# Optimization experiments

Hardware: AMD Instinct MI355X
Metric: run time of the kernel (lower is better)

The kernel has to match this reference:

```python
import jax, jax.numpy as jnp
import numpy as np

CAPACITY_FACTOR = 1.25

def setup_inputs() -> dict:
    key = jax.random.key(0)
    ks = jax.random.split(key, 6)
    B, S, D, H, E = 4, 2048, 1024, 2048, 8
    x = jax.random.normal(ks[0], (B, S, D), dtype=jnp.float32)
    Wg = jax.random.normal(ks[1], (D, E), dtype=jnp.float32) / np.float32(np.sqrt(D))
    bg = jnp.zeros((E,), dtype=jnp.float32)
    W1 = jax.random.normal(ks[2], (E, H, D), dtype=jnp.float32) / np.float32(np.sqrt(H))
    W2 = jax.random.normal(ks[3], (E, D, H), dtype=jnp.float32) / np.float32(np.sqrt(D))
    W3 = jax.random.normal(ks[4], (E, D, H), dtype=jnp.float32) / np.float32(np.sqrt(D))
    return {"x": x, "Wg": Wg, "bg": bg, "W1": W1, "W2": W2, "W3": W3, "deterministic": 1}


def reference(x, Wg, bg, W1, W2, W3, deterministic):
    # deterministic=True path: no gate noise, no dropout (rate=0 anyway).
    b, s, d = x.shape
    E = W1.shape[0]
    xt = x.reshape(-1, d)                      # [N, d]
    N = xt.shape[0]
    cap = int(N / E * CAPACITY_FACTOR)

    logits = xt @ Wg + bg                      # [N, E]
    eid = jnp.argmax(logits, axis=1)           # [N] assigned expert (top-1)
    onehot = jax.nn.one_hot(eid, E, dtype=xt.dtype)
    # 0-based arrival position of each token within its expert's queue
    pos = (jnp.sum(jnp.cumsum(onehot, axis=0) * onehot, axis=1)).astype(jnp.int32) - 1
    valid = pos < cap                          # capacity mask (pos >= 0 always)
    slot = jnp.where(valid, pos, cap)          # overflow tokens -> dummy slot `cap`

    # Dispatch: scatter tokens into [E, cap+1, d]; slots unique among valid tokens
    buf = jnp.zeros((E, cap + 1, d), dtype=xt.dtype).at[eid, slot].set(xt)
    binp = buf[:, :cap]                        # [E, cap, d] (dummy slot dropped)

    # Grouped SwiGLU FFN per expert
    h = jax.nn.silu(jnp.einsum('ecd,edh->ech', binp, W2)) * jnp.einsum('ecd,edh->ech', binp, W3)
    bout = jnp.einsum('ech,ehd->ecd', h, W1)   # [E, cap, d]

    # Combine: gather each token's expert output; overflow tokens read zero row
    bout = jnp.concatenate([bout, jnp.zeros((E, 1, d), dtype=bout.dtype)], axis=1)
    eout = bout[eid, slot]                     # [N, d]

    weights = jax.nn.softmax(logits, axis=-1)
    gate_w = jnp.take_along_axis(weights, eid[:, None], axis=1)  # [N, 1]
    out = (gate_w * eout).reshape(b, s, d)
    return out
```

## Files before the change

### kernel.cpp

```cpp
#include <hip/hip_runtime.h>

#define N_TOK 8192
#define D_DIM 1024
#define H_DIM 2048
#define E_NUM 8
#define CAP   1280

typedef __attribute__((ext_vector_type(8))) short bf16x8;
typedef __attribute__((ext_vector_type(8))) unsigned short u16x8;
typedef __attribute__((ext_vector_type(4))) float f32x4;

__device__ inline unsigned short f2bf(float f) {
  unsigned u = __float_as_uint(f);
  u += 0x7fffu + ((u >> 16) & 1u);
  return (unsigned short)(u >> 16);
}

__device__ inline void vm_drain() {
  asm volatile("s_waitcnt vmcnt(0)" ::: "memory");
}

__global__ __launch_bounds__(256) void transpose_cvt(const float* __restrict__ src,
                                                     unsigned short* __restrict__ dst,
                                                     int R, int C) {
  __shared__ float tile[64][33];
  const int b = blockIdx.z;
  src += (size_t)b * R * C;
  dst += (size_t)b * R * C;
  const int c0 = blockIdx.x * 32, r0 = blockIdx.y * 64;
  const int tx = threadIdx.x & 31, ty = threadIdx.x >> 5;
#pragma unroll
  for (int i = 0; i < 8; ++i)
    tile[ty + i * 8][tx] = src[(size_t)(r0 + ty + i * 8) * C + c0 + tx];
  __syncthreads();
  const int rp = threadIdx.x & 31;
  const int cb = threadIdx.x >> 5;
#pragma unroll
  for (int it = 0; it < 4; ++it) {
    const int c = cb + it * 8;
    unsigned short v[2] = {f2bf(tile[2 * rp][c]), f2bf(tile[2 * rp + 1][c])};
    *reinterpret_cast<unsigned*>(dst + (size_t)(c0 + c) * R + r0 + 2 * rp) =
        *reinterpret_cast<unsigned*>(v);
  }
}

__global__ __launch_bounds__(256) void gate_kernel(const float* __restrict__ x,
                                                   const float* __restrict__ Wg,
                                                   const float* __restrict__ bg,
                                                   int* __restrict__ eid,
                                                   float* __restrict__ gatew) {
  __shared__ float wg[E_NUM][D_DIM];
  const int tid = threadIdx.x;
  for (int i = tid; i < D_DIM * E_NUM; i += 256) {
    int d = i >> 3, e = i & 7;
    wg[e][d] = Wg[i];
  }
  __syncthreads();
  const int w = tid >> 6, l = tid & 63;
  const int t = blockIdx.x * 4 + w;
  const float* xr = x + (size_t)t * D_DIM;
  float acc[8] = {0, 0, 0, 0, 0, 0, 0, 0};
#pragma unroll
  for (int i = 0; i < D_DIM / 64; ++i) {
    float xv = xr[l + 64 * i];
#pragma unroll
    for (int e = 0; e < 8; ++e) acc[e] += xv * wg[e][l + 64 * i];
  }
#pragma unroll
  for (int off = 32; off >= 1; off >>= 1) {
#pragma unroll
    for (int e = 0; e < 8; ++e) acc[e] += __shfl_xor(acc[e], off);
  }
  if (l == 0) {
    float best = -1e30f;
    int bi = 0;
#pragma unroll
    for (int e = 0; e < 8; ++e) {
      acc[e] += bg[e];
      if (acc[e] > best) { best = acc[e]; bi = e; }
    }
    float s = 0.f;
#pragma unroll
    for (int e = 0; e < 8; ++e) s += __expf(acc[e] - best);
    eid[t] = bi;
    gatew[t] = 1.f / s;
  }
}

__global__ void init_tok(int* __restrict__ tok_of) {
  int i = blockIdx.x * 256 + threadIdx.x;
  if (i < E_NUM * CAP) tok_of[i] = -1;
}

__global__ void scan_kernel(const int* __restrict__ eid, int* __restrict__ slot,
                            int* __restrict__ tok_of) {
  __shared__ int se[N_TOK];
  const int tid = threadIdx.x;
  for (int i = tid; i < N_TOK; i += 256) se[i] = eid[i];
  __syncthreads();
  if (tid >= 64) return;
  int counts[8] = {0, 0, 0, 0, 0, 0, 0, 0};
  const unsigned long long lower = (tid == 0) ? 0ull : ((1ull << tid) - 1ull);
  for (int base = 0; base < N_TOK; base += 64) {
    const int t = base + tid;
    const int e = se[t];
    int rank = 0;
#pragma unroll
    for (int ee = 0; ee < 8; ++ee) {
      unsigned long long m = __ballot(e == ee);
      if (e == ee) rank = counts[ee] + __popcll(m & lower);
      counts[ee] += __popcll(m);
    }
    slot[t] = rank < CAP ? rank : CAP;
    if (rank < CAP) tok_of[e * CAP + rank] = t;
  }
}

__global__ __launch_bounds__(256) void scatter_kernel(const float* __restrict__ x,
                                                      const int* __restrict__ tok_of,
                                                      unsigned short* __restrict__ binp) {
  const int row = blockIdx.x * 4 + (threadIdx.x >> 6);
  const int l = threadIdx.x & 63;
  const int t = tok_of[row];
  unsigned short* dst = binp + (size_t)row * D_DIM;
  if (t >= 0) {
    const float* src = x + (size_t)t * D_DIM;
#pragma unroll
    for (int i = 0; i < 4; ++i) {
      const int d = (i * 64 + l) * 4;
      float4 v = *reinterpret_cast<const float4*>(src + d);
      unsigned short r[4] = {f2bf(v.x), f2bf(v.y), f2bf(v.z), f2bf(v.w)};
      *reinterpret_cast<uint2*>(dst + d) = *reinterpret_cast<uint2*>(r);
    }
  } else {
    uint2 z = {0u, 0u};
#pragma unroll
    for (int i = 0; i < 4; ++i) {
      const int d = (i * 64 + l) * 4;
      *reinterpret_cast<uint2*>(dst + d) = z;
    }
  }
}

__device__ inline void stage_tile_async(const unsigned short* __restrict__ g, int ldg, int k0,
                                        unsigned short* lds, int w, int l) {
  const int gcol = (l & 7) ^ (l >> 3);
  const unsigned short* gsrc = g + (size_t)(w * 32 + (l >> 3)) * ldg + k0 + gcol * 8;
#pragma unroll
  for (int it = 0; it < 4; ++it) {
    __builtin_amdgcn_global_load_lds(
        (const __attribute__((address_space(1))) unsigned int*)(gsrc + (size_t)(it * 8) * ldg),
        (__attribute__((address_space(3))) unsigned int*)(lds + (w * 32 + it * 8) * 64),
        16, 0, 0);
  }
}

__device__ inline bf16x8 lds_frag(const unsigned short* lds, int row, int c16) {
  return *reinterpret_cast<const bf16x8*>(lds + row * 64 + (c16 ^ (row & 7)) * 8);
}

__global__ __launch_bounds__(256, 2) void ffn1_kernel(const unsigned short* __restrict__ binp,
                                                      const unsigned short* __restrict__ w2t,
                                                      const unsigned short* __restrict__ w3t,
                                                      unsigned short* __restrict__ hbuf) {
  __shared__ unsigned short sA[128 * 64], sB2[128 * 64], sB3[128 * 64];
  const int e = blockIdx.z;
  const unsigned short* A  = binp + (size_t)e * CAP * D_DIM + (size_t)blockIdx.y * 128 * D_DIM;
  const unsigned short* B2 = w2t + (size_t)e * H_DIM * D_DIM + (size_t)blockIdx.x * 128 * D_DIM;
  const unsigned short* B3 = w3t + (size_t)e * H_DIM * D_DIM + (size_t)blockIdx.x * 128 * D_DIM;
  unsigned short* H = hbuf + (size_t)e * CAP * H_DIM;
  const int tid = threadIdx.x;
  const int l = tid & 63;
  const int w = tid >> 6, wr = w >> 1, wc = w & 1;
  f32x4 acc2[4][4] = {};
  f32x4 acc3[4][4] = {};
  for (int kt = 0; kt < D_DIM / 64; ++kt) {
    __syncthreads();
    stage_tile_async(A, D_DIM, kt * 64, sA, w, l);
    stage_tile_async(B2, D_DIM, kt * 64, sB2, w, l);
    stage_tile_async(B3, D_DIM, kt * 64, sB3, w, l);
    vm_drain();
    __syncthreads();
#pragma unroll
    for (int kk = 0; kk < 2; ++kk) {
      const int c16 = kk * 4 + (l >> 4);
      bf16x8 af[4], b2f[4], b3f[4];
#pragma unroll
      for (int f = 0; f < 4; ++f) {
        af[f] = lds_frag(sA, wr * 64 + f * 16 + (l & 15), c16);
        b2f[f] = lds_frag(sB2, wc * 64 + f * 16 + (l & 15), c16);
        b3f[f] = lds_frag(sB3, wc * 64 + f * 16 + (l & 15), c16);
      }
#pragma unroll
      for (int fm = 0; fm < 4; ++fm)
#pragma unroll
        for (int fn = 0; fn < 4; ++fn) {
          acc2[fm][fn] = __builtin_amdgcn_mfma_f32_16x16x32_bf16(af[fm], b2f[fn], acc2[fm][fn], 0, 0, 0);
          acc3[fm][fn] = __builtin_amdgcn_mfma_f32_16x16x32_bf16(af[fm], b3f[fn], acc3[fm][fn], 0, 0, 0);
        }
    }
  }
  const int row0 = blockIdx.y * 128 + wr * 64;
  const int col0 = blockIdx.x * 128 + wc * 64;
#pragma unroll
  for (int fm = 0; fm < 4; ++fm)
#pragma unroll
    for (int fn = 0; fn < 4; ++fn)
#pragma unroll
      for (int j = 0; j < 4; ++j) {
        const int row = row0 + fm * 16 + (l >> 4) * 4 + j;
        const int col = col0 + fn * 16 + (l & 15);
        const float v1 = acc2[fm][fn][j];
        const float v2 = acc3[fm][fn][j];
        const float hv = (v1 / (1.0f + __expf(-v1))) * v2;
        H[(size_t)row * H_DIM + col] = f2bf(hv);
      }
}

__global__ __launch_bounds__(256, 2) void ffn2_kernel(const unsigned short* __restrict__ hbuf,
                                                      const unsigned short* __restrict__ w1t,
                                                      const int* __restrict__ tok_of,
                                                      const float* __restrict__ gatew,
                                                      float* __restrict__ out) {
  __shared__ unsigned short sA[128 * 64], sB[128 * 64];
  const int e = blockIdx.z;
  const unsigned short* A = hbuf + (size_t)e * CAP * H_DIM + (size_t)blockIdx.y * 128 * H_DIM;
  const unsigned short* B = w1t + (size_t)e * D_DIM * H_DIM + (size_t)blockIdx.x * 128 * H_DIM;
  const int* tok = tok_of + e * CAP;
  const int tid = threadIdx.x;
  const int l = tid & 63;
  const int w = tid >> 6, wr = w >> 1, wc = w & 1;
  f32x4 acc[4][4] = {};
  for (int kt = 0; kt < H_DIM / 64; ++kt) {
    __syncthreads();
    stage_tile_async(A, H_DIM, kt * 64, sA, w, l);
    stage_tile_async(B, H_DIM, kt * 64, sB, w, l);
    vm_drain();
    __syncthreads();
#pragma unroll
    for (int kk = 0; kk < 2; ++kk) {
      const int c16 = kk * 4 + (l >> 4);
      bf16x8 af[4], bf[4];
#pragma unroll
      for (int f = 0; f < 4; ++f) {
        af[f] = lds_frag(sA, wr * 64 + f * 16 + (l & 15), c16);
        bf[f] = lds_frag(sB, wc * 64 + f * 16 + (l & 15), c16);
      }
#pragma unroll
      for (int fm = 0; fm < 4; ++fm)
#pragma unroll
        for (int fn = 0; fn < 4; ++fn)
          acc[fm][fn] = __builtin_amdgcn_mfma_f32_16x16x32_bf16(af[fm], bf[fn], acc[fm][fn], 0, 0, 0);
    }
  }
  const int row0 = blockIdx.y * 128 + wr * 64;
  const int col0 = blockIdx.x * 128 + wc * 64;
#pragma unroll
  for (int fm = 0; fm < 4; ++fm)
#pragma unroll
    for (int j = 0; j < 4; ++j) {
      const int row = row0 + fm * 16 + (l >> 4) * 4 + j;
      const int t = tok[row];
      if (t >= 0) {
        const float g = gatew[t];
#pragma unroll
        for (int fn = 0; fn < 4; ++fn) {
          const int col = col0 + fn * 16 + (l & 15);
          out[(size_t)t * D_DIM + col] = g * acc[fm][fn][j];
        }
      }
    }
}

__global__ __launch_bounds__(256) void zero_overflow(const int* __restrict__ slot,
                                                     float* __restrict__ out) {
  const int t = blockIdx.x * 4 + (threadIdx.x >> 6);
  if (slot[t] < CAP) return;
  const int l = threadIdx.x & 63;
  float4 z = {0.f, 0.f, 0.f, 0.f};
#pragma unroll
  for (int i = 0; i < 4; ++i)
    *reinterpret_cast<float4*>(out + (size_t)t * D_DIM + (i * 64 + l) * 4) = z;
}

extern "C" void kernel_launch(void* const* d_in, const int* in_sizes, int n_in,
                              void* d_out, int out_size, void* d_ws, size_t ws_size,
                              hipStream_t stream) {
  const float* x  = (const float*)d_in[0];
  const float* Wg = (const float*)d_in[1];
  const float* bg = (const float*)d_in[2];
  const float* W1 = (const float*)d_in[3];
  const float* W2 = (const float*)d_in[4];
  const float* W3 = (const float*)d_in[5];
  float* out = (float*)d_out;

  char* ws = (char*)d_ws;
  unsigned short* w2t = (unsigned short*)ws; ws += (size_t)E_NUM * H_DIM * D_DIM * 2;
  unsigned short* w3t = (unsigned short*)ws; ws += (size_t)E_NUM * H_DIM * D_DIM * 2;
  unsigned short* w1t = (unsigned short*)ws; ws += (size_t)E_NUM * D_DIM * H_DIM * 2;
  unsigned short* binp = (unsigned short*)ws; ws += (size_t)E_NUM * CAP * D_DIM * 2;
  unsigned short* hbuf = (unsigned short*)ws; ws += (size_t)E_NUM * CAP * H_DIM * 2;
  int* eid = (int*)ws;    ws += (size_t)N_TOK * 4;
  float* gw = (float*)ws; ws += (size_t)N_TOK * 4;
  int* slot = (int*)ws;   ws += (size_t)N_TOK * 4;
  int* tok_of = (int*)ws; ws += (size_t)E_NUM * CAP * 4;

  dim3 tb(256);
  transpose_cvt<<<dim3(H_DIM / 32, D_DIM / 64, E_NUM), tb, 0, stream>>>(W2, w2t, D_DIM, H_DIM);
  transpose_cvt<<<dim3(H_DIM / 32, D_DIM / 64, E_NUM), tb, 0, stream>>>(W3, w3t, D_DIM, H_DIM);
  transpose_cvt<<<dim3(D_DIM / 32, H_DIM / 64, E_NUM), tb, 0, stream>>>(W1, w1t, H_DIM, D_DIM);

  init_tok<<<(E_NUM * CAP + 255) / 256, 256, 0, stream>>>(tok_of);
  gate_kernel<<<N_TOK / 4, 256, 0, stream>>>(x, Wg, bg, eid, gw);
  scan_kernel<<<1, 256, 0, stream>>>(eid, slot, tok_of);
  scatter_kernel<<<E_NUM * CAP / 4, 256, 0, stream>>>(x, tok_of, binp);
  ffn1_kernel<<<dim3(H_DIM / 128, CAP / 128, E_NUM), 256, 0, stream>>>(binp, w2t, w3t, hbuf);
  ffn2_kernel<<<dim3(D_DIM / 128, CAP / 128, E_NUM), 256, 0, stream>>>(hbuf, w1t, tok_of, gw, out);
  zero_overflow<<<N_TOK / 4, 256, 0, stream>>>(slot, out);
}
```

Measured before the change: 272.7 us.

## Prefetch next A tile in FFN GEMMs and merge weight transposes into one launch

Both FFN GEMM kernels now double-buffer the activation (A) tile in LDS. The next A tile is prefetched while the current one is consumed, and a partial vmcnt wait plus raw s_barrier replace the full drain. The three weight transpose/convert launches become one kernel that splits on block index, and the init_tok kernel is replaced by hipMemsetAsync. The aim is to hide part of the global-load latency and cut launch overhead. B tiles stay single-buffered, so their load latency remains exposed, and the extra LDS buffer may reduce occupancy.

```diff
diff --git a/kernel.cpp b/kernel.cpp
--- a/kernel.cpp
+++ b/kernel.cpp
@@ -7,7 +7,6 @@
 #define CAP   1280
 
 typedef __attribute__((ext_vector_type(8))) short bf16x8;
-typedef __attribute__((ext_vector_type(8))) unsigned short u16x8;
 typedef __attribute__((ext_vector_type(4))) float f32x4;
 
 __device__ inline unsigned short f2bf(float f) {
@@ -16,18 +15,41 @@
   return (unsigned short)(u >> 16);
 }
 
-__device__ inline void vm_drain() {
-  asm volatile("s_waitcnt vmcnt(0)" ::: "memory");
-}
-
-__global__ __launch_bounds__(256) void transpose_cvt(const float* __restrict__ src,
-                                                     unsigned short* __restrict__ dst,
-                                                     int R, int C) {
+#define VMCNT(n) asm volatile("s_waitcnt vmcnt(" #n ")" ::: "memory")
+#define BARRIER() asm volatile("s_barrier" ::: "memory")
+
+__global__ __launch_bounds__(256) void transpose_cvt_all(const float* __restrict__ W2,
+                                                         const float* __restrict__ W3,
+                                                         const float* __restrict__ W1,
+                                                         unsigned short* __restrict__ w2t,
+                                                         unsigned short* __restrict__ w3t,
+                                                         unsigned short* __restrict__ w1t) {
   __shared__ float tile[64][33];
-  const int b = blockIdx.z;
+  const int id = blockIdx.x;
+  const float* src;
+  unsigned short* dst;
+  int R, C, bx, by, b;
+  if (id < 16384) {
+    const int q = id & 8191;
+    b = q >> 10;
+    const int rem = q & 1023;
+    bx = rem & 63;
+    by = rem >> 6;
+    R = D_DIM; C = H_DIM;
+    src = (id < 8192 ? W2 : W3);
+    dst = (id < 8192 ? w2t : w3t);
+  } else {
+    const int q = id - 16384;
+    b = q >> 10;
+    const int rem = q & 1023;
+    bx = rem & 31;
+    by = rem >> 5;
+    R = H_DIM; C = D_DIM;
+    src = W1; dst = w1t;
+  }
   src += (size_t)b * R * C;
   dst += (size_t)b * R * C;
-  const int c0 = blockIdx.x * 32, r0 = blockIdx.y * 64;
+  const int c0 = bx * 32, r0 = by * 64;
   const int tx = threadIdx.x & 31, ty = threadIdx.x >> 5;
 #pragma unroll
   for (int i = 0; i < 8; ++i)
@@ -85,11 +107,6 @@
     eid[t] = bi;
     gatew[t] = 1.f / s;
   }
-}
-
-__global__ void init_tok(int* __restrict__ tok_of) {
-  int i = blockIdx.x * 256 + threadIdx.x;
-  if (i < E_NUM * CAP) tok_of[i] = -1;
 }
 
 __global__ void scan_kernel(const int* __restrict__ eid, int* __restrict__ slot,
@@ -142,8 +159,10 @@
   }
 }
 
-__device__ inline void stage_tile_async(const unsigned short* __restrict__ g, int ldg, int k0,
-                                        unsigned short* lds, int w, int l) {
+#define TILE64 (128 * 64)
+
+__device__ inline void stage_tile(const unsigned short* __restrict__ g, int ldg, int k0,
+                                  unsigned short* lds, int w, int l) {
   const int gcol = (l & 7) ^ (l >> 3);
   const unsigned short* gsrc = g + (size_t)(w * 32 + (l >> 3)) * ldg + k0 + gcol * 8;
 #pragma unroll
@@ -163,31 +182,39 @@
                                                       const unsigned short* __restrict__ w2t,
                                                       const unsigned short* __restrict__ w3t,
                                                       unsigned short* __restrict__ hbuf) {
-  __shared__ unsigned short sA[128 * 64], sB2[128 * 64], sB3[128 * 64];
-  const int e = blockIdx.z;
-  const unsigned short* A  = binp + (size_t)e * CAP * D_DIM + (size_t)blockIdx.y * 128 * D_DIM;
-  const unsigned short* B2 = w2t + (size_t)e * H_DIM * D_DIM + (size_t)blockIdx.x * 128 * D_DIM;
-  const unsigned short* B3 = w3t + (size_t)e * H_DIM * D_DIM + (size_t)blockIdx.x * 128 * D_DIM;
+  __shared__ unsigned short sA[2][TILE64], sB2[TILE64], sB3[TILE64];
+  const int e = blockIdx.z, bx = blockIdx.x, by = blockIdx.y;
+  const unsigned short* A  = binp + (size_t)e * CAP * D_DIM + (size_t)by * 128 * D_DIM;
+  const unsigned short* B2 = w2t + (size_t)e * H_DIM * D_DIM + (size_t)bx * 128 * D_DIM;
+  const unsigned short* B3 = w3t + (size_t)e * H_DIM * D_DIM + (size_t)bx * 128 * D_DIM;
   unsigned short* H = hbuf + (size_t)e * CAP * H_DIM;
   const int tid = threadIdx.x;
   const int l = tid & 63;
   const int w = tid >> 6, wr = w >> 1, wc = w & 1;
   f32x4 acc2[4][4] = {};
   f32x4 acc3[4][4] = {};
-  for (int kt = 0; kt < D_DIM / 64; ++kt) {
-    __syncthreads();
-    stage_tile_async(A, D_DIM, kt * 64, sA, w, l);
-    stage_tile_async(B2, D_DIM, kt * 64, sB2, w, l);
-    stage_tile_async(B3, D_DIM, kt * 64, sB3, w, l);
-    vm_drain();
-    __syncthreads();
+
+  stage_tile(A, D_DIM, 0, sA[0], w, l);
+
+  const int NT = D_DIM / 64;
+  int cur = 0;
+  for (int kt = 0; kt < NT; ++kt) {
+    stage_tile(B2, D_DIM, kt * 64, sB2, w, l);
+    stage_tile(B3, D_DIM, kt * 64, sB3, w, l);
+    if (kt + 1 < NT) {
+      stage_tile(A, D_DIM, (kt + 1) * 64, sA[cur ^ 1], w, l);
+      VMCNT(4);
+    } else {
+      VMCNT(0);
+    }
+    BARRIER();
 #pragma unroll
     for (int kk = 0; kk < 2; ++kk) {
       const int c16 = kk * 4 + (l >> 4);
       bf16x8 af[4], b2f[4], b3f[4];
 #pragma unroll
       for (int f = 0; f < 4; ++f) {
-        af[f] = lds_frag(sA, wr * 64 + f * 16 + (l & 15), c16);
+        af[f]  = lds_frag(sA[cur], wr * 64 + f * 16 + (l & 15), c16);
         b2f[f] = lds_frag(sB2, wc * 64 + f * 16 + (l & 15), c16);
         b3f[f] = lds_frag(sB3, wc * 64 + f * 16 + (l & 15), c16);
       }
@@ -199,9 +226,12 @@
           acc3[fm][fn] = __builtin_amdgcn_mfma_f32_16x16x32_bf16(af[fm], b3f[fn], acc3[fm][fn], 0, 0, 0);
         }
     }
-  }
-  const int row0 = blockIdx.y * 128 + wr * 64;
-  const int col0 = blockIdx.x * 128 + wc * 64;
+    BARRIER();
+    cur ^= 1;
+  }
+
+  const int row0 = by * 128 + wr * 64;
+  const int col0 = bx * 128 + wc * 64;
 #pragma unroll
   for (int fm = 0; fm < 4; ++fm)
 #pragma unroll
@@ -210,9 +240,9 @@
       for (int j = 0; j < 4; ++j) {
         const int row = row0 + fm * 16 + (l >> 4) * 4 + j;
         const int col = col0 + fn * 16 + (l & 15);
-        const float v1 = acc2[fm][fn][j];
-        const float v2 = acc3[fm][fn][j];
-        const float hv = (v1 / (1.0f + __expf(-v1))) * v2;
+        const float v2 = acc2[fm][fn][j];
+        const float v3 = acc3[fm][fn][j];
+        const float hv = (v2 / (1.0f + __expf(-v2))) * v3;
         H[(size_t)row * H_DIM + col] = f2bf(hv);
       }
 }
@@ -222,7 +252,7 @@
                                                       const int* __restrict__ tok_of,
                                                       const float* __restrict__ gatew,
                                                       float* __restrict__ out) {
-  __shared__ unsigned short sA[128 * 64], sB[128 * 64];
+  __shared__ unsigned short sA[2][TILE64], sB[TILE64];
   const int e = blockIdx.z;
   const unsigned short* A = hbuf + (size_t)e * CAP * H_DIM + (size_t)blockIdx.y * 128 * H_DIM;
   const unsigned short* B = w1t + (size_t)e * D_DIM * H_DIM + (size_t)blockIdx.x * 128 * H_DIM;
@@ -231,28 +261,39 @@
   const int l = tid & 63;
   const int w = tid >> 6, wr = w >> 1, wc = w & 1;
   f32x4 acc[4][4] = {};
-  for (int kt = 0; kt < H_DIM / 64; ++kt) {
-    __syncthreads();
-    stage_tile_async(A, H_DIM, kt * 64, sA, w, l);
-    stage_tile_async(B, H_DIM, kt * 64, sB, w, l);
-    vm_drain();
-    __syncthreads();
+
+  stage_tile(A, H_DIM, 0, sA[0], w, l);
+
+  const int NT = H_DIM / 64;
+  int cur = 0;
+  for (int kt = 0; kt < NT; ++kt) {
+    stage_tile(B, H_DIM, kt * 64, sB, w, l);
+    if (kt + 1 < NT) {
+      stage_tile(A, H_DIM, (kt + 1) * 64, sA[cur ^ 1], w, l);
+      VMCNT(4);
+    } else {
+      VMCNT(0);
+    }
+    BARRIER();
 #pragma unroll
     for (int kk = 0; kk < 2; ++kk) {
       const int c16 = kk * 4 + (l >> 4);
-      bf16x8 af[4], bf[4];
+      bf16x8 af[4], bfr[4];
 #pragma unroll
       for (int f = 0; f < 4; ++f) {
-        af[f] = lds_frag(sA, wr * 64 + f * 16 + (l & 15), c16);
-        bf[f] = lds_frag(sB, wc * 64 + f * 16 + (l & 15), c16);
+        af[f]  = lds_frag(sA[cur], wr * 64 + f * 16 + (l & 15), c16);
+        bfr[f] = lds_frag(sB, wc * 64 + f * 16 + (l & 15), c16);
       }
 #pragma unroll
       for (int fm = 0; fm < 4; ++fm)
 #pragma unroll
         for (int fn = 0; fn < 4; ++fn)
-          acc[fm][fn] = __builtin_amdgcn_mfma_f32_16x16x32_bf16(af[fm], bf[fn], acc[fm][fn], 0, 0, 0);
-    }
-  }
+          acc[fm][fn] = __builtin_amdgcn_mfma_f32_16x16x32_bf16(af[fm], bfr[fn], acc[fm][fn], 0, 0, 0);
+    }
+    BARRIER();
+    cur ^= 1;
+  }
+
   const int row0 = blockIdx.y * 128 + wr * 64;
   const int col0 = blockIdx.x * 128 + wc * 64;
 #pragma unroll
@@ -305,12 +346,8 @@
   int* slot = (int*)ws;   ws += (size_t)N_TOK * 4;
   int* tok_of = (int*)ws; ws += (size_t)E_NUM * CAP * 4;
 
-  dim3 tb(256);
-  transpose_cvt<<<dim3(H_DIM / 32, D_DIM / 64, E_NUM), tb, 0, stream>>>(W2, w2t, D_DIM, H_DIM);
-  transpose_cvt<<<dim3(H_DIM / 32, D_DIM / 64, E_NUM), tb, 0, stream>>>(W3, w3t, D_DIM, H_DIM);
-  transpose_cvt<<<dim3(D_DIM / 32, H_DIM / 64, E_NUM), tb, 0, stream>>>(W1, w1t, H_DIM, D_DIM);
-
-  init_tok<<<(E_NUM * CAP + 255) / 256, 256, 0, stream>>>(tok_of);
+  transpose_cvt_all<<<24576, 256, 0, stream>>>(W2, W3, W1, w2t, w3t, w1t);
+  hipMemsetAsync(tok_of, 0xFF, (size_t)E_NUM * CAP * 4, stream);
   gate_kernel<<<N_TOK / 4, 256, 0, stream>>>(x, Wg, bg, eid, gw);
   scan_kernel<<<1, 256, 0, stream>>>(eid, slot, tok_of);
   scatter_kernel<<<E_NUM * CAP / 4, 256, 0, stream>>>(x, tok_of, binp);
```

Result: faster. 264.9 us (-2.9%).
